# Optimization experiments

Measured on AMD Instinct MI355X. Metric: run time of the kernel, lower is better.

Reference implementation:

```python
import jax, jax.numpy as jnp
import numpy as np

B, T, F, H = 4096, 128, 64, 32
SCALE = 0.05  # small init so relu-LSTM doesn't blow up over 128 steps


def setup_inputs() -> dict:
    key = jax.random.key(0)
    ks = jax.random.split(key, 7)
    return {
        "x": jax.random.normal(ks[0], (B, T, F), jnp.float32),
        "We": jax.random.normal(ks[1], (F, 4 * H), jnp.float32) * SCALE,
        "Ue": jax.random.normal(ks[2], (H, 4 * H), jnp.float32) * SCALE,
        "be": jnp.zeros((4 * H,), jnp.float32),
        "Wd": jax.random.normal(ks[3], (H, 4 * H), jnp.float32) * SCALE,
        "Ud": jax.random.normal(ks[4], (H, 4 * H), jnp.float32) * SCALE,
        "bd": jnp.zeros((4 * H,), jnp.float32),
        "Wout": jax.random.normal(ks[5], (H, F), jnp.float32) * SCALE,
        "bout": jnp.zeros((F,), jnp.float32),
    }


def _lstm_relu(x, W, U, b):
    """Keras LSTM with activation='relu', recurrent_activation='sigmoid'.
    x: [B,T,D]. Returns (h_T [B,H], h_seq [B,T,H]). Gate order: i,f,c,o."""
    Bx = x.shape[0]
    Hh = U.shape[0]
    xz = jnp.einsum('btd,dg->btg', x, W) + b  # precompute input projections

    def step(carry, zt):
        h, c = carry
        z = zt + h @ U
        i, f, g, o = jnp.split(z, 4, axis=-1)
        i = jax.nn.sigmoid(i)
        f = jax.nn.sigmoid(f)
        g = jax.nn.relu(g)
        o = jax.nn.sigmoid(o)
        c = f * c + i * g
        h = o * jax.nn.relu(c)
        return (h, c), h

    h0 = jnp.zeros((Bx, Hh), x.dtype)
    (hT, _), hs = jax.lax.scan(step, (h0, h0), jnp.swapaxes(xz, 0, 1))
    return hT, jnp.swapaxes(hs, 0, 1)


def reference(x, We, Ue, be, Wd, Ud, bd, Wout, bout):
    # Encoder: LSTM(32, relu, return_sequences=False) -> RepeatVector(T)
    hT, _ = _lstm_relu(x, We, Ue, be)                      # [B,H]
    z = jnp.broadcast_to(hT[:, None, :], (x.shape[0], x.shape[1], hT.shape[-1]))
    # Decoder: LSTM(32, relu, return_sequences=True) -> TimeDistributed(Dense(F))
    _, hs = _lstm_relu(z, Wd, Ud, bd)                      # [B,T,H]
    return jnp.einsum('bth,hf->btf', hs, Wout) + bout      # [B,T,F]
```

## Files before the change

### kernel.cpp

```cpp
#include <hip/hip_runtime.h>
#include <hip/hip_bf16.h>

#define B_ 4096
#define T_ 128
#define F_ 64
#define H_ 32
#define G_ 128

using short8 = __attribute__((ext_vector_type(8))) short;
using f32x4  = __attribute__((ext_vector_type(4))) float;

#define MFMA16(Af, Bf, Cf) __builtin_amdgcn_mfma_f32_16x16x32_bf16((Af), (Bf), (Cf), 0, 0, 0)

__device__ __forceinline__ float sigmoid_f(float z) {
    return __builtin_amdgcn_rcpf(1.0f + __expf(-z));
}
__device__ __forceinline__ unsigned short bfb(float f) {
    return __builtin_bit_cast(unsigned short, __float2bfloat16(f));
}

extern "C" __global__ __launch_bounds__(64, 1)
void lstm_ae(const float* __restrict__ x,
             const float* __restrict__ We,
             const float* __restrict__ Ue,
             const float* __restrict__ be,
             const float* __restrict__ Wd,
             const float* __restrict__ Ud,
             const float* __restrict__ bd,
             const float* __restrict__ Wout,
             const float* __restrict__ bout,
             float* __restrict__ out)
{
    const int lane = threadIdx.x;
    const int g = lane >> 4;
    const int c = lane & 15;
    const int b0 = blockIdx.x << 4;

    short8 weF[8][2];
    short8 ueF[8];
#pragma unroll
    for (int n = 0; n < 8; ++n) {
#pragma unroll
        for (int kc = 0; kc < 2; ++kc)
#pragma unroll
            for (int i = 0; i < 8; ++i)
                weF[n][kc][i] = (short)bfb(We[(kc * 32 + 8 * g + i) * G_ + 16 * n + c]);
#pragma unroll
        for (int i = 0; i < 8; ++i)
            ueF[n][i] = (short)bfb(Ue[(4 * g + (i & 3) + 16 * (i >> 2)) * G_ + 16 * n + c]);
    }
    f32x4 beC[8];
#pragma unroll
    for (int n = 0; n < 8; ++n)
        beC[n] = *(const f32x4*)(be + 16 * n + 4 * g);

    const float* xr = x + (size_t)(b0 + c) * (T_ * F_);
    const int xo = 8 * g;

    short8 hfrag = (short8)0;
    float cs[2][4];
#pragma unroll
    for (int jh = 0; jh < 2; ++jh)
#pragma unroll
        for (int r = 0; r < 4; ++r) cs[jh][r] = 0.f;

    f32x4 xa = *(const f32x4*)(xr + xo);
    f32x4 xb = *(const f32x4*)(xr + xo + 4);
    f32x4 xc = *(const f32x4*)(xr + 32 + xo);
    f32x4 xd = *(const f32x4*)(xr + 36 + xo);

#pragma unroll 1
    for (int t = 0; t < T_; ++t) {
        short8 xf0, xf1;
#pragma unroll
        for (int i = 0; i < 4; ++i) {
            xf0[i]     = (short)bfb(xa[i]);
            xf0[4 + i] = (short)bfb(xb[i]);
            xf1[i]     = (short)bfb(xc[i]);
            xf1[4 + i] = (short)bfb(xd[i]);
        }
        if (t + 1 < T_) {
            const float* xn = xr + (t + 1) * F_;
            xa = *(const f32x4*)(xn + xo);
            xb = *(const f32x4*)(xn + xo + 4);
            xc = *(const f32x4*)(xn + 32 + xo);
            xd = *(const f32x4*)(xn + 36 + xo);
        }

        f32x4 acc[8];
#pragma unroll
        for (int n = 0; n < 8; ++n) {
            acc[n] = MFMA16(weF[n][0], xf0, beC[n]);
            acc[n] = MFMA16(weF[n][1], xf1, acc[n]);
            acc[n] = MFMA16(ueF[n], hfrag, acc[n]);
        }

#pragma unroll
        for (int jh = 0; jh < 2; ++jh)
#pragma unroll
            for (int r = 0; r < 4; ++r) {
                float iv = sigmoid_f(acc[0 + jh][r]);
                float fv = sigmoid_f(acc[2 + jh][r]);
                float gv = fmaxf(acc[4 + jh][r], 0.f);
                float ov = sigmoid_f(acc[6 + jh][r]);
                float cc = fmaf(fv, cs[jh][r], iv * gv);
                cs[jh][r] = cc;
                float hv = ov * fmaxf(cc, 0.f);
                hfrag[4 * jh + r] = (short)bfb(hv);
            }
    }

    short8 udF[8], woF[4];
    f32x4 zd[8], boC[4];
    {
        short8 wdF[8];
#pragma unroll
        for (int n = 0; n < 8; ++n)
#pragma unroll
            for (int i = 0; i < 8; ++i) {
                int pr = 4 * g + (i & 3) + 16 * (i >> 2);
                wdF[n][i] = (short)bfb(Wd[pr * G_ + 16 * n + c]);
                udF[n][i] = (short)bfb(Ud[pr * G_ + 16 * n + c]);
            }
#pragma unroll
        for (int m = 0; m < 4; ++m) {
#pragma unroll
            for (int i = 0; i < 8; ++i)
                woF[m][i] = (short)bfb(Wout[(4 * g + (i & 3) + 16 * (i >> 2)) * F_ + 16 * m + c]);
            float v = bout[16 * m + c];
            f32x4 tb; tb[0] = v; tb[1] = v; tb[2] = v; tb[3] = v;
            boC[m] = tb;
        }
#pragma unroll
        for (int n = 0; n < 8; ++n) {
            f32x4 tb = *(const f32x4*)(bd + 16 * n + 4 * g);
            zd[n] = MFMA16(wdF[n], hfrag, tb);
        }
    }

    hfrag = (short8)0;
#pragma unroll
    for (int jh = 0; jh < 2; ++jh)
#pragma unroll
        for (int r = 0; r < 4; ++r) cs[jh][r] = 0.f;

    float* ob[4];
#pragma unroll
    for (int r = 0; r < 4; ++r)
        ob[r] = out + (size_t)(b0 + 4 * g + r) * (T_ * F_) + c;

#pragma unroll 1
    for (int t = 0; t < T_; ++t) {
        f32x4 acc[8];
#pragma unroll
        for (int n = 0; n < 8; ++n)
            acc[n] = MFMA16(udF[n], hfrag, zd[n]);

#pragma unroll
        for (int jh = 0; jh < 2; ++jh)
#pragma unroll
            for (int r = 0; r < 4; ++r) {
                float iv = sigmoid_f(acc[0 + jh][r]);
                float fv = sigmoid_f(acc[2 + jh][r]);
                float gv = fmaxf(acc[4 + jh][r], 0.f);
                float ov = sigmoid_f(acc[6 + jh][r]);
                float cc = fmaf(fv, cs[jh][r], iv * gv);
                cs[jh][r] = cc;
                float hv = ov * fmaxf(cc, 0.f);
                hfrag[4 * jh + r] = (short)bfb(hv);
            }

        f32x4 oac[4];
#pragma unroll
        for (int m = 0; m < 4; ++m)
            oac[m] = MFMA16(hfrag, woF[m], boC[m]);
#pragma unroll
        for (int m = 0; m < 4; ++m)
#pragma unroll
            for (int r = 0; r < 4; ++r)
                ob[r][t * F_ + 16 * m] = oac[m][r];
    }
}

extern "C" void kernel_launch(void* const* d_in, const int* in_sizes, int n_in,
                              void* d_out, int out_size, void* d_ws, size_t ws_size,
                              hipStream_t stream) {
    (void)in_sizes; (void)n_in; (void)d_ws; (void)ws_size; (void)out_size;
    const float* x    = (const float*)d_in[0];
    const float* We   = (const float*)d_in[1];
    const float* Ue   = (const float*)d_in[2];
    const float* be   = (const float*)d_in[3];
    const float* Wd   = (const float*)d_in[4];
    const float* Ud   = (const float*)d_in[5];
    const float* bd   = (const float*)d_in[6];
    const float* Wout = (const float*)d_in[7];
    const float* bout = (const float*)d_in[8];
    float* out = (float*)d_out;

    dim3 grid(B_ / 16), block(64);
    hipLaunchKernelGGL(lstm_ae, grid, block, 0, stream,
                       x, We, Ue, be, Wd, Ud, bd, Wout, bout, out);
}
```

Baseline: 404.4 us.

## Split LSTM gate columns across two waves with LDS hidden-state exchange

Each 16-row batch tile is now handled by two wavefronts instead of one. Each wave computes half of the gate column tiles, which is the hidden units for its half. The two waves swap packed bf16 hidden values through double-buffered shared memory with a barrier every timestep, and the output projection is also split between the waves. This halves the serial per-step MFMA and activation work per wave to shorten the recurrence critical path. The cost is a per-step __syncthreads and an LDS round trip, and there are only 256 blocks.

```diff
diff --git a/kernel.cpp b/kernel.cpp
--- a/kernel.cpp
+++ b/kernel.cpp
@@ -9,6 +9,8 @@
 
 using short8 = __attribute__((ext_vector_type(8))) short;
 using f32x4  = __attribute__((ext_vector_type(4))) float;
+using uint2v = __attribute__((ext_vector_type(2))) unsigned int;
+using uint4v = __attribute__((ext_vector_type(4))) unsigned int;
 
 #define MFMA16(Af, Bf, Cf) __builtin_amdgcn_mfma_f32_16x16x32_bf16((Af), (Bf), (Cf), 0, 0, 0)
 
@@ -18,8 +20,11 @@
 __device__ __forceinline__ unsigned short bfb(float f) {
     return __builtin_bit_cast(unsigned short, __float2bfloat16(f));
 }
-
-extern "C" __global__ __launch_bounds__(64, 1)
+__device__ __forceinline__ unsigned int pk(float a, float b) {
+    return (unsigned int)bfb(a) | ((unsigned int)bfb(b) << 16);
+}
+
+extern "C" __global__ __launch_bounds__(128, 1)
 void lstm_ae(const float* __restrict__ x,
              const float* __restrict__ We,
              const float* __restrict__ Ue,
@@ -31,38 +36,38 @@
              const float* __restrict__ bout,
              float* __restrict__ out)
 {
-    const int lane = threadIdx.x;
-    const int g = lane >> 4;
-    const int c = lane & 15;
-    const int b0 = blockIdx.x << 4;
-
-    short8 weF[8][2];
-    short8 ueF[8];
-#pragma unroll
-    for (int n = 0; n < 8; ++n) {
+    const int lane = threadIdx.x & 63;
+    const int w    = threadIdx.x >> 6;
+    const int g    = lane >> 4;
+    const int c    = lane & 15;
+    const int b0   = blockIdx.x << 4;
+
+    __shared__ __align__(16) unsigned int hx[2][16][18];
+
+    short8 weF[4][2];
+    short8 ueF[4];
+    f32x4  beC[4];
+#pragma unroll
+    for (int q = 0; q < 4; ++q) {
+        const int n = 2 * q + w;
 #pragma unroll
         for (int kc = 0; kc < 2; ++kc)
 #pragma unroll
             for (int i = 0; i < 8; ++i)
-                weF[n][kc][i] = (short)bfb(We[(kc * 32 + 8 * g + i) * G_ + 16 * n + c]);
+                weF[q][kc][i] = (short)bfb(We[(kc * 32 + 8 * g + i) * G_ + 16 * n + c]);
 #pragma unroll
         for (int i = 0; i < 8; ++i)
-            ueF[n][i] = (short)bfb(Ue[(4 * g + (i & 3) + 16 * (i >> 2)) * G_ + 16 * n + c]);
-    }
-    f32x4 beC[8];
-#pragma unroll
-    for (int n = 0; n < 8; ++n)
-        beC[n] = *(const f32x4*)(be + 16 * n + 4 * g);
+            ueF[q][i] = (short)bfb(Ue[(4 * g + (i & 3) + 16 * (i >> 2)) * G_ + 16 * n + c]);
+        beC[q] = *(const f32x4*)(be + 16 * n + 4 * g);
+    }
 
     const float* xr = x + (size_t)(b0 + c) * (T_ * F_);
     const int xo = 8 * g;
 
     short8 hfrag = (short8)0;
-    float cs[2][4];
-#pragma unroll
-    for (int jh = 0; jh < 2; ++jh)
-#pragma unroll
-        for (int r = 0; r < 4; ++r) cs[jh][r] = 0.f;
+    float cs[4];
+#pragma unroll
+    for (int r = 0; r < 4; ++r) cs[r] = 0.f;
 
     f32x4 xa = *(const f32x4*)(xr + xo);
     f32x4 xb = *(const f32x4*)(xr + xo + 4);
@@ -87,62 +92,71 @@
             xd = *(const f32x4*)(xn + 36 + xo);
         }
 
-        f32x4 acc[8];
-#pragma unroll
-        for (int n = 0; n < 8; ++n) {
-            acc[n] = MFMA16(weF[n][0], xf0, beC[n]);
-            acc[n] = MFMA16(weF[n][1], xf1, acc[n]);
-            acc[n] = MFMA16(ueF[n], hfrag, acc[n]);
-        }
-
-#pragma unroll
-        for (int jh = 0; jh < 2; ++jh)
-#pragma unroll
-            for (int r = 0; r < 4; ++r) {
-                float iv = sigmoid_f(acc[0 + jh][r]);
-                float fv = sigmoid_f(acc[2 + jh][r]);
-                float gv = fmaxf(acc[4 + jh][r], 0.f);
-                float ov = sigmoid_f(acc[6 + jh][r]);
-                float cc = fmaf(fv, cs[jh][r], iv * gv);
-                cs[jh][r] = cc;
-                float hv = ov * fmaxf(cc, 0.f);
-                hfrag[4 * jh + r] = (short)bfb(hv);
+        f32x4 acc[4];
+#pragma unroll
+        for (int q = 0; q < 4; ++q) {
+            acc[q] = MFMA16(weF[q][0], xf0, beC[q]);
+            acc[q] = MFMA16(weF[q][1], xf1, acc[q]);
+            acc[q] = MFMA16(ueF[q], hfrag, acc[q]);
+        }
+
+        float hv[4];
+#pragma unroll
+        for (int r = 0; r < 4; ++r) {
+            float iv = sigmoid_f(acc[0][r]);
+            float fv = sigmoid_f(acc[1][r]);
+            float gv = fmaxf(acc[2][r], 0.f);
+            float ov = sigmoid_f(acc[3][r]);
+            float cc = fmaf(fv, cs[r], iv * gv);
+            cs[r] = cc;
+            hv[r] = ov * fmaxf(cc, 0.f);
+        }
+        uint2v own; own.x = pk(hv[0], hv[1]); own.y = pk(hv[2], hv[3]);
+        *(uint2v*)&hx[t & 1][c][8 * w + 2 * g] = own;
+        __syncthreads();
+        uint2v oth = *(const uint2v*)&hx[t & 1][c][8 * (1 - w) + 2 * g];
+        uint4v hb;
+        hb.x = w ? oth.x : own.x;
+        hb.y = w ? oth.y : own.y;
+        hb.z = w ? own.x : oth.x;
+        hb.w = w ? own.y : oth.y;
+        hfrag = __builtin_bit_cast(short8, hb);
+    }
+
+    short8 udF[4], woF[2];
+    f32x4  zd[4], boC[2];
+    {
+        short8 wdF[4];
+#pragma unroll
+        for (int q = 0; q < 4; ++q) {
+            const int n = 2 * q + w;
+#pragma unroll
+            for (int i = 0; i < 8; ++i) {
+                const int pr = 4 * g + (i & 3) + 16 * (i >> 2);
+                wdF[q][i] = (short)bfb(Wd[pr * G_ + 16 * n + c]);
+                udF[q][i] = (short)bfb(Ud[pr * G_ + 16 * n + c]);
             }
-    }
-
-    short8 udF[8], woF[4];
-    f32x4 zd[8], boC[4];
-    {
-        short8 wdF[8];
-#pragma unroll
-        for (int n = 0; n < 8; ++n)
-#pragma unroll
-            for (int i = 0; i < 8; ++i) {
-                int pr = 4 * g + (i & 3) + 16 * (i >> 2);
-                wdF[n][i] = (short)bfb(Wd[pr * G_ + 16 * n + c]);
-                udF[n][i] = (short)bfb(Ud[pr * G_ + 16 * n + c]);
-            }
-#pragma unroll
-        for (int m = 0; m < 4; ++m) {
+        }
+#pragma unroll
+        for (int mi = 0; mi < 2; ++mi) {
+            const int m = 2 * w + mi;
 #pragma unroll
             for (int i = 0; i < 8; ++i)
-                woF[m][i] = (short)bfb(Wout[(4 * g + (i & 3) + 16 * (i >> 2)) * F_ + 16 * m + c]);
+                woF[mi][i] = (short)bfb(Wout[(4 * g + (i & 3) + 16 * (i >> 2)) * F_ + 16 * m + c]);
             float v = bout[16 * m + c];
             f32x4 tb; tb[0] = v; tb[1] = v; tb[2] = v; tb[3] = v;
-            boC[m] = tb;
-        }
-#pragma unroll
-        for (int n = 0; n < 8; ++n) {
-            f32x4 tb = *(const f32x4*)(bd + 16 * n + 4 * g);
-            zd[n] = MFMA16(wdF[n], hfrag, tb);
+            boC[mi] = tb;
+        }
+#pragma unroll
+        for (int q = 0; q < 4; ++q) {
+            f32x4 tb = *(const f32x4*)(bd + 16 * (2 * q + w) + 4 * g);
+            zd[q] = MFMA16(wdF[q], hfrag, tb);
         }
     }
 
     hfrag = (short8)0;
 #pragma unroll
-    for (int jh = 0; jh < 2; ++jh)
-#pragma unroll
-        for (int r = 0; r < 4; ++r) cs[jh][r] = 0.f;
+    for (int r = 0; r < 4; ++r) cs[r] = 0.f;
 
     float* ob[4];
 #pragma unroll
@@ -151,34 +165,41 @@
 
 #pragma unroll 1
     for (int t = 0; t < T_; ++t) {
-        f32x4 acc[8];
-#pragma unroll
-        for (int n = 0; n < 8; ++n)
-            acc[n] = MFMA16(udF[n], hfrag, zd[n]);
-
-#pragma unroll
-        for (int jh = 0; jh < 2; ++jh)
-#pragma unroll
-            for (int r = 0; r < 4; ++r) {
-                float iv = sigmoid_f(acc[0 + jh][r]);
-                float fv = sigmoid_f(acc[2 + jh][r]);
-                float gv = fmaxf(acc[4 + jh][r], 0.f);
-                float ov = sigmoid_f(acc[6 + jh][r]);
-                float cc = fmaf(fv, cs[jh][r], iv * gv);
-                cs[jh][r] = cc;
-                float hv = ov * fmaxf(cc, 0.f);
-                hfrag[4 * jh + r] = (short)bfb(hv);
-            }
-
-        f32x4 oac[4];
-#pragma unroll
-        for (int m = 0; m < 4; ++m)
-            oac[m] = MFMA16(hfrag, woF[m], boC[m]);
-#pragma unroll
-        for (int m = 0; m < 4; ++m)
+        f32x4 acc[4];
+#pragma unroll
+        for (int q = 0; q < 4; ++q)
+            acc[q] = MFMA16(udF[q], hfrag, zd[q]);
+
+        float hv[4];
+#pragma unroll
+        for (int r = 0; r < 4; ++r) {
+            float iv = sigmoid_f(acc[0][r]);
+            float fv = sigmoid_f(acc[1][r]);
+            float gv = fmaxf(acc[2][r], 0.f);
+            float ov = sigmoid_f(acc[3][r]);
+            float cc = fmaf(fv, cs[r], iv * gv);
+            cs[r] = cc;
+            hv[r] = ov * fmaxf(cc, 0.f);
+        }
+        uint2v own; own.x = pk(hv[0], hv[1]); own.y = pk(hv[2], hv[3]);
+        *(uint2v*)&hx[t & 1][c][8 * w + 2 * g] = own;
+        __syncthreads();
+        uint2v oth = *(const uint2v*)&hx[t & 1][c][8 * (1 - w) + 2 * g];
+        uint4v hb;
+        hb.x = w ? oth.x : own.x;
+        hb.y = w ? oth.y : own.y;
+        hb.z = w ? own.x : oth.x;
+        hb.w = w ? own.y : oth.y;
+        hfrag = __builtin_bit_cast(short8, hb);
+
+#pragma unroll
+        for (int mi = 0; mi < 2; ++mi) {
+            f32x4 oac = MFMA16(hfrag, woF[mi], boC[mi]);
+            const int m = 2 * w + mi;
 #pragma unroll
             for (int r = 0; r < 4; ++r)
-                ob[r][t * F_ + 16 * m] = oac[m][r];
+                ob[r][t * F_ + 16 * m] = oac[r];
+        }
     }
 }
 
@@ -197,7 +218,7 @@
     const float* bout = (const float*)d_in[8];
     float* out = (float*)d_out;
 
-    dim3 grid(B_ / 16), block(64);
+    dim3 grid(B_ / 16), block(128);
     hipLaunchKernelGGL(lstm_ae, grid, block, 0, stream,
                        x, We, Ue, be, Wd, Ud, bd, Wout, bout, out);
 }
```

After: 345.6 us. 14.5% less time.

## Split LSTM gate math across four waves per block with LDS hidden-state exchange

Applied to the files above, without the earlier changes.

Each block now runs four wavefronts that all compute the same gate MFMAs redundantly. Each wave evaluates the nonlinearities for only one of the four accumulator rows, packs its two bf16 h values, and exchanges them through a double-buffered shared-memory array with a barrier every timestep. The output projection is also split so each wave computes one 16-column slice. The aim is to cut the serial per-step elementwise latency, at the cost of redundant MFMA work, a block-wide sync per step, and fewer blocks able to run per CU.

```diff
diff --git a/kernel.cpp b/kernel.cpp
--- a/kernel.cpp
+++ b/kernel.cpp
@@ -9,6 +9,7 @@
 
 using short8 = __attribute__((ext_vector_type(8))) short;
 using f32x4  = __attribute__((ext_vector_type(4))) float;
+using uint4v = __attribute__((ext_vector_type(4))) unsigned int;
 
 #define MFMA16(Af, Bf, Cf) __builtin_amdgcn_mfma_f32_16x16x32_bf16((Af), (Bf), (Cf), 0, 0, 0)
 
@@ -18,8 +19,30 @@
 __device__ __forceinline__ unsigned short bfb(float f) {
     return __builtin_bit_cast(unsigned short, __float2bfloat16(f));
 }
-
-extern "C" __global__ __launch_bounds__(64, 1)
+__device__ __forceinline__ unsigned int pk(float a, float b) {
+    return (unsigned int)bfb(a) | ((unsigned int)bfb(b) << 16);
+}
+
+#define GATES(R)                                              \
+    {                                                         \
+        float iv0 = sigmoid_f(acc[0][R]);                     \
+        float fv0 = sigmoid_f(acc[2][R]);                     \
+        float gv0 = fmaxf(acc[4][R], 0.f);                    \
+        float ov0 = sigmoid_f(acc[6][R]);                     \
+        float cc0 = fmaf(fv0, cs0, iv0 * gv0);                \
+        cs0 = cc0;                                            \
+        float h0 = ov0 * fmaxf(cc0, 0.f);                     \
+        float iv1 = sigmoid_f(acc[1][R]);                     \
+        float fv1 = sigmoid_f(acc[3][R]);                     \
+        float gv1 = fmaxf(acc[5][R], 0.f);                    \
+        float ov1 = sigmoid_f(acc[7][R]);                     \
+        float cc1 = fmaf(fv1, cs1, iv1 * gv1);                \
+        cs1 = cc1;                                            \
+        float h1 = ov1 * fmaxf(cc1, 0.f);                     \
+        hword = pk(h0, h1);                                   \
+    }
+
+extern "C" __global__ __launch_bounds__(256, 1)
 void lstm_ae(const float* __restrict__ x,
              const float* __restrict__ We,
              const float* __restrict__ Ue,
@@ -31,13 +54,17 @@
              const float* __restrict__ bout,
              float* __restrict__ out)
 {
-    const int lane = threadIdx.x;
-    const int g = lane >> 4;
-    const int c = lane & 15;
-    const int b0 = blockIdx.x << 4;
+    const int lane = threadIdx.x & 63;
+    const int w    = threadIdx.x >> 6;
+    const int g    = lane >> 4;
+    const int c    = lane & 15;
+    const int b0   = blockIdx.x << 4;
+
+    __shared__ __align__(16) unsigned int hx[2][16 * 20];
 
     short8 weF[8][2];
     short8 ueF[8];
+    f32x4  beC[8];
 #pragma unroll
     for (int n = 0; n < 8; ++n) {
 #pragma unroll
@@ -47,22 +74,15 @@
                 weF[n][kc][i] = (short)bfb(We[(kc * 32 + 8 * g + i) * G_ + 16 * n + c]);
 #pragma unroll
         for (int i = 0; i < 8; ++i)
-            ueF[n][i] = (short)bfb(Ue[(4 * g + (i & 3) + 16 * (i >> 2)) * G_ + 16 * n + c]);
-    }
-    f32x4 beC[8];
-#pragma unroll
-    for (int n = 0; n < 8; ++n)
+            ueF[n][i] = (short)bfb(Ue[(4 * g + (i >> 1) + 16 * (i & 1)) * G_ + 16 * n + c]);
         beC[n] = *(const f32x4*)(be + 16 * n + 4 * g);
+    }
 
     const float* xr = x + (size_t)(b0 + c) * (T_ * F_);
     const int xo = 8 * g;
 
     short8 hfrag = (short8)0;
-    float cs[2][4];
-#pragma unroll
-    for (int jh = 0; jh < 2; ++jh)
-#pragma unroll
-        for (int r = 0; r < 4; ++r) cs[jh][r] = 0.f;
+    float cs0 = 0.f, cs1 = 0.f;
 
     f32x4 xa = *(const f32x4*)(xr + xo);
     f32x4 xb = *(const f32x4*)(xr + xo + 4);
@@ -95,59 +115,53 @@
             acc[n] = MFMA16(ueF[n], hfrag, acc[n]);
         }
 
-#pragma unroll
-        for (int jh = 0; jh < 2; ++jh)
-#pragma unroll
-            for (int r = 0; r < 4; ++r) {
-                float iv = sigmoid_f(acc[0 + jh][r]);
-                float fv = sigmoid_f(acc[2 + jh][r]);
-                float gv = fmaxf(acc[4 + jh][r], 0.f);
-                float ov = sigmoid_f(acc[6 + jh][r]);
-                float cc = fmaf(fv, cs[jh][r], iv * gv);
-                cs[jh][r] = cc;
-                float hv = ov * fmaxf(cc, 0.f);
-                hfrag[4 * jh + r] = (short)bfb(hv);
-            }
-    }
-
-    short8 udF[8], woF[4];
-    f32x4 zd[8], boC[4];
+        unsigned int hword;
+        switch (w) {
+            case 0: GATES(0) break;
+            case 1: GATES(1) break;
+            case 2: GATES(2) break;
+            default: GATES(3) break;
+        }
+        hx[t & 1][c * 20 + 4 * g + w] = hword;
+        __syncthreads();
+        hfrag = __builtin_bit_cast(short8, *(const uint4v*)&hx[t & 1][c * 20 + 4 * g]);
+    }
+
+    short8 udF[8];
+    f32x4  zd[8];
     {
         short8 wdF[8];
 #pragma unroll
         for (int n = 0; n < 8; ++n)
 #pragma unroll
             for (int i = 0; i < 8; ++i) {
-                int pr = 4 * g + (i & 3) + 16 * (i >> 2);
+                const int pr = 4 * g + (i >> 1) + 16 * (i & 1);
                 wdF[n][i] = (short)bfb(Wd[pr * G_ + 16 * n + c]);
                 udF[n][i] = (short)bfb(Ud[pr * G_ + 16 * n + c]);
             }
 #pragma unroll
-        for (int m = 0; m < 4; ++m) {
-#pragma unroll
-            for (int i = 0; i < 8; ++i)
-                woF[m][i] = (short)bfb(Wout[(4 * g + (i & 3) + 16 * (i >> 2)) * F_ + 16 * m + c]);
-            float v = bout[16 * m + c];
-            f32x4 tb; tb[0] = v; tb[1] = v; tb[2] = v; tb[3] = v;
-            boC[m] = tb;
-        }
-#pragma unroll
         for (int n = 0; n < 8; ++n) {
             f32x4 tb = *(const f32x4*)(bd + 16 * n + 4 * g);
             zd[n] = MFMA16(wdF[n], hfrag, tb);
         }
     }
+    short8 woF;
+    f32x4  boC;
+    {
+#pragma unroll
+        for (int i = 0; i < 8; ++i)
+            woF[i] = (short)bfb(Wout[(4 * g + (i >> 1) + 16 * (i & 1)) * F_ + 16 * w + c]);
+        float v = bout[16 * w + c];
+        boC[0] = v; boC[1] = v; boC[2] = v; boC[3] = v;
+    }
 
     hfrag = (short8)0;
-#pragma unroll
-    for (int jh = 0; jh < 2; ++jh)
-#pragma unroll
-        for (int r = 0; r < 4; ++r) cs[jh][r] = 0.f;
+    cs0 = 0.f; cs1 = 0.f;
 
     float* ob[4];
 #pragma unroll
     for (int r = 0; r < 4; ++r)
-        ob[r] = out + (size_t)(b0 + 4 * g + r) * (T_ * F_) + c;
+        ob[r] = out + (size_t)(b0 + 4 * g + r) * (T_ * F_) + 16 * w + c;
 
 #pragma unroll 1
     for (int t = 0; t < T_; ++t) {
@@ -156,29 +170,21 @@
         for (int n = 0; n < 8; ++n)
             acc[n] = MFMA16(udF[n], hfrag, zd[n]);
 
-#pragma unroll
-        for (int jh = 0; jh < 2; ++jh)
-#pragma unroll
-            for (int r = 0; r < 4; ++r) {
-                float iv = sigmoid_f(acc[0 + jh][r]);
-                float fv = sigmoid_f(acc[2 + jh][r]);
-                float gv = fmaxf(acc[4 + jh][r], 0.f);
-                float ov = sigmoid_f(acc[6 + jh][r]);
-                float cc = fmaf(fv, cs[jh][r], iv * gv);
-                cs[jh][r] = cc;
-                float hv = ov * fmaxf(cc, 0.f);
-                hfrag[4 * jh + r] = (short)bfb(hv);
-            }
-
-        f32x4 oac[4];
-#pragma unroll
-        for (int m = 0; m < 4; ++m)
-            oac[m] = MFMA16(hfrag, woF[m], boC[m]);
-#pragma unroll
-        for (int m = 0; m < 4; ++m)
-#pragma unroll
-            for (int r = 0; r < 4; ++r)
-                ob[r][t * F_ + 16 * m] = oac[m][r];
+        unsigned int hword;
+        switch (w) {
+            case 0: GATES(0) break;
+            case 1: GATES(1) break;
+            case 2: GATES(2) break;
+            default: GATES(3) break;
+        }
+        hx[t & 1][c * 20 + 4 * g + w] = hword;
+        __syncthreads();
+        hfrag = __builtin_bit_cast(short8, *(const uint4v*)&hx[t & 1][c * 20 + 4 * g]);
+
+        f32x4 oac = MFMA16(hfrag, woF, boC);
+#pragma unroll
+        for (int r = 0; r < 4; ++r)
+            ob[r][t * F_] = oac[r];
     }
 }
 
@@ -197,7 +203,7 @@
     const float* bout = (const float*)d_in[8];
     float* out = (float*)d_out;
 
-    dim3 grid(B_ / 16), block(64);
+    dim3 grid(B_ / 16), block(256);
     hipLaunchKernelGGL(lstm_ae, grid, block, 0, stream,
                        x, We, Ue, be, Wd, Ud, bd, Wout, bout, out);
 }
```

Result: slower. 422.7 us (+4.5%).
